# Optimization experiments

Measured on AMD Instinct MI355X. Metric: run time of the kernel, lower is better.

The kernel has to match this reference:

```python
import jax, jax.numpy as jnp
import numpy as np

BLOCK_LEN = 64

def _exp_segsum(cs):
    # cs: (..., T) cumulative sums; out[..., i, j] = exp(cs_i - cs_j) for i>=j else 0
    T = cs.shape[-1]
    diff = cs[..., :, None] - cs[..., None, :]
    mask = jnp.tril(jnp.ones((T, T), dtype=bool))
    return jnp.where(mask, jnp.exp(diff), 0.0)

def setup_inputs() -> dict:
    key = jax.random.key(0)
    k1, k2, k3, k4 = jax.random.split(key, 4)
    b, s, h, p, n = 16, 4096, 16, 64, 64
    X = jax.random.normal(k1, (b, s, h, p), jnp.float32)
    # decay-like A (negative, small magnitude) so exp(segsum) is numerically bounded
    A = -jnp.abs(jax.random.normal(k2, (b, s, h), jnp.float32)) * 0.05
    B = jax.random.normal(k3, (b, s, h, n), jnp.float32)
    C = jax.random.normal(k4, (b, s, h, n), jnp.float32)
    return {"X": X, "A": A, "B": B, "C": C}

def reference(X, A, B, C):
    b, s, h, p = X.shape
    n = B.shape[-1]
    l = BLOCK_LEN
    c = s // l
    # chunk into blocks: b (c l) ... -> b c l ...
    Xb = X.reshape(b, c, l, h, p)
    Ab = A.reshape(b, c, l, h)
    Bb = B.reshape(b, c, l, h, n)
    # Cb = C.reshape(b, c, l, h, n)  # original computes Y_diag with C but discards it
    # A cumsum per chunk: (b, h, c, l)
    A_cs = jnp.cumsum(jnp.transpose(Ab, (0, 3, 1, 2)), axis=-1)
    # intra-chunk states: decay to end of chunk, reduce over l
    decay = jnp.exp(A_cs[..., -1:] - A_cs)  # (b, h, c, l)
    states = jnp.einsum('bclhn,bhcl,bclhp->bchpn', Bb, decay, Xb)  # (b,c,h,p,n)
    # prepend zero initial state
    init = jnp.zeros_like(states[:, :1])
    states = jnp.concatenate([init, states], axis=1)  # (b, c+1, h, p, n)
    # inter-chunk decay matrix from per-chunk total sums
    chunk_sum = jnp.pad(A_cs[..., -1], ((0, 0), (0, 0), (1, 0)))  # (b, h, c+1)
    decay_chunk = _exp_segsum(jnp.cumsum(chunk_sum, axis=-1))  # (b, h, c+1, c+1)
    new_states = jnp.einsum('bhzc,bchpn->bzhpn', decay_chunk, states)
    return new_states[:, -1]  # (b, h, p, n)
```

## Files before the change

### kernel.cpp

```cpp
#include <hip/hip_runtime.h>

constexpr int S  = 4096;
constexpr int H  = 16;
constexpr int P  = 64;
constexpr int NN = 64;
constexpr int PAIRS = 256;
constexpr int KSPLIT = 8;
constexpr int TT = 16;
constexpr float WMIN = 1e-12f;

__global__ __launch_bounds__(256) void scan_w(const float* __restrict__ A,
                                              float* __restrict__ w) {
    const int pair = blockIdx.x;
    const int b = pair >> 4, h = pair & 15;
    const float* Ab = A + (size_t)b * S * H + h;
    const int j = threadIdx.x;

    float a[16];
    float lsum = 0.f;
#pragma unroll
    for (int i = 0; i < 16; ++i) {
        a[i] = Ab[(size_t)(j * 16 + i) * H];
        lsum += a[i];
    }

    __shared__ float sd[256];
    sd[j] = lsum;
    __syncthreads();
    float incl = lsum;
    for (int off = 1; off < 256; off <<= 1) {
        float add = (j >= off) ? sd[j - off] : 0.f;
        __syncthreads();
        incl += add;
        sd[j] = incl;
        __syncthreads();
    }
    const float total = sd[255];
    float run = incl - lsum;

    float* wrow = w + (size_t)pair * S + j * 16;
#pragma unroll
    for (int i = 0; i < 16; ++i) {
        run += a[i];
        wrow[i] = expf(total - run);
    }
}

__global__ __launch_bounds__(256) void mainK(const float* __restrict__ X,
                                             const float* __restrict__ Bm,
                                             const float* __restrict__ w,
                                             float* __restrict__ out) {
    const int pair = blockIdx.x;
    const int ks   = blockIdx.y;
    const int b = pair >> 4, h = pair & 15;
    const int tid = threadIdx.x;

    const float* wrow = w + (size_t)pair * S;

    __shared__ int si[256];
    si[tid] = (wrow[(size_t)tid * 16] >= WMIN) ? tid : 256;
    __syncthreads();
    for (int off = 128; off > 0; off >>= 1) {
        if (tid < off) si[tid] = min(si[tid], si[tid + off]);
        __syncthreads();
    }
    const int m = si[0];
    const int c0 = (m >= 256) ? (S - TT) : ((m > 0) ? (m - 1) * TT : 0);

    const int nTiles = (S - c0) >> 4;
    const int tpb = (nTiles + KSPLIT - 1) / KSPLIT;
    const int i0 = ks * tpb;
    const int i1 = min(nTiles, i0 + tpb);
    if (i0 >= i1) return;

    const float* Xp = X  + (size_t)b * S * H * P  + (size_t)h * P;
    const float* Bp = Bm + (size_t)b * S * H * NN + (size_t)h * NN;

    __shared__ float Xs[TT][P];
    __shared__ float Bs[TT][NN];

    const int row = tid >> 4;
    const int c4  = (tid & 15) * 4;
    const int tp  = (tid >> 4) * 4;
    const int tn  = (tid & 15) * 4;

    float acc[4][4];
#pragma unroll
    for (int i = 0; i < 4; ++i)
#pragma unroll
        for (int j = 0; j < 4; ++j) acc[i][j] = 0.f;

    int t = c0 + i0 * TT + row;
    float  wv = wrow[t];
    float4 xv = *(const float4*)(Xp + (size_t)t * (H * P)  + c4);
    float4 bv = *(const float4*)(Bp + (size_t)t * (H * NN) + c4);

    for (int i = i0; i < i1; ++i) {
        __syncthreads();
        *(float4*)(&Xs[row][c4]) = make_float4(xv.x * wv, xv.y * wv, xv.z * wv, xv.w * wv);
        *(float4*)(&Bs[row][c4]) = bv;
        __syncthreads();

        if (i + 1 < i1) {
            t = c0 + (i + 1) * TT + row;
            wv = wrow[t];
            xv = *(const float4*)(Xp + (size_t)t * (H * P)  + c4);
            bv = *(const float4*)(Bp + (size_t)t * (H * NN) + c4);
        }

#pragma unroll
        for (int r = 0; r < TT; ++r) {
            const float4 xr = *(const float4*)(&Xs[r][tp]);
            const float4 br = *(const float4*)(&Bs[r][tn]);
            const float xa[4] = {xr.x, xr.y, xr.z, xr.w};
            const float ba[4] = {br.x, br.y, br.z, br.w};
#pragma unroll
            for (int ii = 0; ii < 4; ++ii)
#pragma unroll
                for (int jj = 0; jj < 4; ++jj)
                    acc[ii][jj] = fmaf(xa[ii], ba[jj], acc[ii][jj]);
        }
    }

    float* op = out + (size_t)pair * (P * NN);
#pragma unroll
    for (int i = 0; i < 4; ++i)
#pragma unroll
        for (int j = 0; j < 4; ++j)
            atomicAdd(&op[(size_t)(tp + i) * NN + tn + j], acc[i][j]);
}

extern "C" void kernel_launch(void* const* d_in, const int* in_sizes, int n_in,
                              void* d_out, int out_size, void* d_ws, size_t ws_size,
                              hipStream_t stream) {
    const float* X = (const float*)d_in[0];
    const float* A = (const float*)d_in[1];
    const float* B = (const float*)d_in[2];
    float* out = (float*)d_out;
    float* w   = (float*)d_ws;

    hipMemsetAsync(d_out, 0, (size_t)out_size * sizeof(float), stream);
    scan_w<<<PAIRS, 256, 0, stream>>>(A, w);
    mainK<<<dim3(PAIRS, KSPLIT), 256, 0, stream>>>(X, B, w, out);
}
```

Measured before the change: 612.5 us.

## Compute skip cutoff in scan kernel and use 8x8 register tiles with split-K waves

The scan kernel now records, per (batch, head), the first timestep whose decay weight exceeds the threshold, so the main kernel no longer runs its own reduction. The main kernel drops to 128 threads, each owning an 8x8 accumulator tile. The two waves each take half of the 16-row tile, and their partial sums are combined through shared memory before the atomics. Shared rows are padded to reduce bank conflicts. The intent is more FMAs per shared-memory load and fewer atomics, at the cost of higher register pressure and fewer threads per block.

```diff
diff --git a/kernel.cpp b/kernel.cpp
--- a/kernel.cpp
+++ b/kernel.cpp
@@ -7,10 +7,12 @@
 constexpr int PAIRS = 256;
 constexpr int KSPLIT = 8;
 constexpr int TT = 16;
+constexpr int LDP = 72;
 constexpr float WMIN = 1e-12f;
 
 __global__ __launch_bounds__(256) void scan_w(const float* __restrict__ A,
-                                              float* __restrict__ w) {
+                                              float* __restrict__ w,
+                                              int* __restrict__ cut) {
     const int pair = blockIdx.x;
     const int b = pair >> 4, h = pair & 15;
     const float* Ab = A + (size_t)b * S * H + h;
@@ -25,6 +27,7 @@
     }
 
     __shared__ float sd[256];
+    __shared__ int   ci[256];
     sd[j] = lsum;
     __syncthreads();
     float incl = lsum;
@@ -39,33 +42,39 @@
     float run = incl - lsum;
 
     float* wrow = w + (size_t)pair * S + j * 16;
+    int firstIdx = S;
 #pragma unroll
     for (int i = 0; i < 16; ++i) {
         run += a[i];
-        wrow[i] = expf(total - run);
+        const float wv = expf(total - run);
+        wrow[i] = wv;
+        if (wv >= WMIN && firstIdx == S) firstIdx = j * 16 + i;
     }
+
+    ci[j] = firstIdx;
+    __syncthreads();
+    for (int off = 128; off > 0; off >>= 1) {
+        if (j < off) ci[j] = min(ci[j], ci[j + off]);
+        __syncthreads();
+    }
+    if (j == 0) cut[pair] = ci[0];
 }
 
-__global__ __launch_bounds__(256) void mainK(const float* __restrict__ X,
-                                             const float* __restrict__ Bm,
-                                             const float* __restrict__ w,
-                                             float* __restrict__ out) {
+__global__ __launch_bounds__(128, 4) void mainK(const float* __restrict__ X,
+                                                const float* __restrict__ Bm,
+                                                const float* __restrict__ w,
+                                                const int* __restrict__ cut,
+                                                float* __restrict__ out) {
     const int pair = blockIdx.x;
     const int ks   = blockIdx.y;
     const int b = pair >> 4, h = pair & 15;
-    const int tid = threadIdx.x;
+    const int tid  = threadIdx.x;
+    const int wave = tid >> 6;
+    const int lane = tid & 63;
 
     const float* wrow = w + (size_t)pair * S;
 
-    __shared__ int si[256];
-    si[tid] = (wrow[(size_t)tid * 16] >= WMIN) ? tid : 256;
-    __syncthreads();
-    for (int off = 128; off > 0; off >>= 1) {
-        if (tid < off) si[tid] = min(si[tid], si[tid + off]);
-        __syncthreads();
-    }
-    const int m = si[0];
-    const int c0 = (m >= 256) ? (S - TT) : ((m > 0) ? (m - 1) * TT : 0);
+    const int c0 = min(S - TT, cut[pair] & ~(TT - 1));
 
     const int nTiles = (S - c0) >> 4;
     const int tpb = (nTiles + KSPLIT - 1) / KSPLIT;
@@ -76,58 +85,82 @@
     const float* Xp = X  + (size_t)b * S * H * P  + (size_t)h * P;
     const float* Bp = Bm + (size_t)b * S * H * NN + (size_t)h * NN;
 
-    __shared__ float Xs[TT][P];
-    __shared__ float Bs[TT][NN];
+    __shared__ float smem[2 * TT * LDP];
+    float* Xs = smem;
+    float* Bs = smem + TT * LDP;
 
-    const int row = tid >> 4;
-    const int c4  = (tid & 15) * 4;
-    const int tp  = (tid >> 4) * 4;
-    const int tn  = (tid & 15) * 4;
+    const int sr = tid >> 3;
+    const int c8 = (tid & 7) * 8;
 
-    float acc[4][4];
+    const int tp = (lane >> 3) * 8;
+    const int tn = (lane & 7) * 8;
+    const int r0 = wave * 8;
+
+    float acc[64];
 #pragma unroll
-    for (int i = 0; i < 4; ++i)
-#pragma unroll
-        for (int j = 0; j < 4; ++j) acc[i][j] = 0.f;
+    for (int k = 0; k < 64; ++k) acc[k] = 0.f;
 
-    int t = c0 + i0 * TT + row;
-    float  wv = wrow[t];
-    float4 xv = *(const float4*)(Xp + (size_t)t * (H * P)  + c4);
-    float4 bv = *(const float4*)(Bp + (size_t)t * (H * NN) + c4);
+    int t = c0 + i0 * TT + sr;
+    float  wv  = wrow[t];
+    float4 xa0 = *(const float4*)(Xp + (size_t)t * (H * P)  + c8);
+    float4 xa1 = *(const float4*)(Xp + (size_t)t * (H * P)  + c8 + 4);
+    float4 ba0 = *(const float4*)(Bp + (size_t)t * (H * NN) + c8);
+    float4 ba1 = *(const float4*)(Bp + (size_t)t * (H * NN) + c8 + 4);
 
     for (int i = i0; i < i1; ++i) {
         __syncthreads();
-        *(float4*)(&Xs[row][c4]) = make_float4(xv.x * wv, xv.y * wv, xv.z * wv, xv.w * wv);
-        *(float4*)(&Bs[row][c4]) = bv;
+        *(float4*)(&Xs[sr * LDP + c8])     = make_float4(xa0.x * wv, xa0.y * wv, xa0.z * wv, xa0.w * wv);
+        *(float4*)(&Xs[sr * LDP + c8 + 4]) = make_float4(xa1.x * wv, xa1.y * wv, xa1.z * wv, xa1.w * wv);
+        *(float4*)(&Bs[sr * LDP + c8])     = ba0;
+        *(float4*)(&Bs[sr * LDP + c8 + 4]) = ba1;
         __syncthreads();
 
         if (i + 1 < i1) {
-            t = c0 + (i + 1) * TT + row;
-            wv = wrow[t];
-            xv = *(const float4*)(Xp + (size_t)t * (H * P)  + c4);
-            bv = *(const float4*)(Bp + (size_t)t * (H * NN) + c4);
+            t = c0 + (i + 1) * TT + sr;
+            wv  = wrow[t];
+            xa0 = *(const float4*)(Xp + (size_t)t * (H * P)  + c8);
+            xa1 = *(const float4*)(Xp + (size_t)t * (H * P)  + c8 + 4);
+            ba0 = *(const float4*)(Bp + (size_t)t * (H * NN) + c8);
+            ba1 = *(const float4*)(Bp + (size_t)t * (H * NN) + c8 + 4);
         }
 
 #pragma unroll
-        for (int r = 0; r < TT; ++r) {
-            const float4 xr = *(const float4*)(&Xs[r][tp]);
-            const float4 br = *(const float4*)(&Bs[r][tn]);
-            const float xa[4] = {xr.x, xr.y, xr.z, xr.w};
-            const float ba[4] = {br.x, br.y, br.z, br.w};
+        for (int r8 = 0; r8 < 8; ++r8) {
+            const int r = r0 + r8;
+            const float4 x0 = *(const float4*)(&Xs[r * LDP + tp]);
+            const float4 x1 = *(const float4*)(&Xs[r * LDP + tp + 4]);
+            const float4 b0 = *(const float4*)(&Bs[r * LDP + tn]);
+            const float4 b1 = *(const float4*)(&Bs[r * LDP + tn + 4]);
+            const float xa[8] = {x0.x, x0.y, x0.z, x0.w, x1.x, x1.y, x1.z, x1.w};
+            const float ba[8] = {b0.x, b0.y, b0.z, b0.w, b1.x, b1.y, b1.z, b1.w};
 #pragma unroll
-            for (int ii = 0; ii < 4; ++ii)
+            for (int ii = 0; ii < 8; ++ii)
 #pragma unroll
-                for (int jj = 0; jj < 4; ++jj)
-                    acc[ii][jj] = fmaf(xa[ii], ba[jj], acc[ii][jj]);
+                for (int jj = 0; jj < 8; ++jj)
+                    acc[ii * 8 + jj] = fmaf(xa[ii], ba[jj], acc[ii * 8 + jj]);
         }
     }
 
-    float* op = out + (size_t)pair * (P * NN);
 #pragma unroll
-    for (int i = 0; i < 4; ++i)
+    for (int c = 0; c < 2; ++c) {
+        __syncthreads();
+        if (wave == 1) {
 #pragma unroll
-        for (int j = 0; j < 4; ++j)
-            atomicAdd(&op[(size_t)(tp + i) * NN + tn + j], acc[i][j]);
+            for (int k = 0; k < 32; ++k) smem[k * 64 + lane] = acc[c * 32 + k];
+        }
+        __syncthreads();
+        if (wave == 0) {
+#pragma unroll
+            for (int k = 0; k < 32; ++k) acc[c * 32 + k] += smem[k * 64 + lane];
+        }
+    }
+
+    if (wave == 0) {
+        float* op = out + (size_t)pair * (P * NN);
+#pragma unroll
+        for (int k = 0; k < 64; ++k)
+            atomicAdd(&op[(size_t)(tp + (k >> 3)) * NN + tn + (k & 7)], acc[k]);
+    }
 }
 
 extern "C" void kernel_launch(void* const* d_in, const int* in_sizes, int n_in,
@@ -138,8 +171,9 @@
     const float* B = (const float*)d_in[2];
     float* out = (float*)d_out;
     float* w   = (float*)d_ws;
+    int*   cut = (int*)((char*)d_ws + (size_t)PAIRS * S * sizeof(float));
 
     hipMemsetAsync(d_out, 0, (size_t)out_size * sizeof(float), stream);
-    scan_w<<<PAIRS, 256, 0, stream>>>(A, w);
-    mainK<<<dim3(PAIRS, KSPLIT), 256, 0, stream>>>(X, B, w, out);
+    scan_w<<<PAIRS, 256, 0, stream>>>(A, w, cut);
+    mainK<<<dim3(PAIRS, KSPLIT), 128, 0, stream>>>(X, B, w, cut, out);
 }
```

Result: slower. 815.3 us (+33.1%).
